# Kernel tuning notes

Measured on AMD Instinct MI355X. Metric: run time of the kernel, lower is better.

## Reference

```python
import jax, jax.numpy as jnp
import numpy as np

LORA_DIM = 16          # hard-coded in module
LORA_TOKEN_INDEX = 1   # lora_dim*layer_sequence + 1 with layer_sequence=0
B, S, D, H = 4, 2048, 1024, 4096  # num_hiddens = 4*num_input (forced by view())


def setup_inputs() -> dict:
    key = jax.random.key(0)
    ks = jax.random.split(key, 6)
    x = jax.random.normal(ks[0], (B, S, D), dtype=jnp.float32)
    W1 = jax.random.normal(ks[1], (H, D), dtype=jnp.float32) * 0.02
    b1 = jnp.zeros((H,), dtype=jnp.float32)
    W2 = jax.random.normal(ks[2], (D, H), dtype=jnp.float32) * 0.02
    b2 = jnp.zeros((D,), dtype=jnp.float32)
    scale = jnp.asarray(0.001, dtype=jnp.float32)  # nn.Parameter(torch.tensor(0.001))
    return {"x": x, "W1": W1, "b1": b1, "W2": W2, "b2": b2, "scale": scale}


def reference(x, W1, b1, W2, b2, scale):
    Bx, Sx, Dx = x.shape
    Hx = W1.shape[0]  # = 4*Dx
    # 16 lora tokens starting at LORA_TOKEN_INDEX
    lt = jax.lax.dynamic_slice_in_dim(x, LORA_TOKEN_INDEX, LORA_DIM, axis=1)
    even = lt[:, ::2, :]  # (B, 8, D)
    odd = lt[:, 1::2, :]  # (B, 8, D)
    # per-sample low-rank weight updates:
    # result_multiplication[b,k] = outer(even[b,k], odd[b,k]) (D,D)
    # matrix1 = first 4 blocks stacked -> (B, 4D, D); matrix2 = last 4 reshaped -> (B, D, 4D)
    m1 = (even[:, :4, :, None] * odd[:, :4, None, :]).reshape(Bx, Hx, Dx)
    m2 = (even[:, 4:, :, None] * odd[:, 4:, None, :]).reshape(Bx, Dx, Hx)
    # x @ (W1 + scale*m1)^T + b1, fused without repeating W1 per batch
    h = jnp.einsum('bsd,hd->bsh', x, W1) + scale * jnp.einsum('bsd,bhd->bsh', x, m1) + b1
    h = jax.nn.gelu(h, approximate=False)  # torch nn.GELU default = exact erf
    out = jnp.einsum('bsh,oh->bso', h, W2) + scale * jnp.einsum('bsh,boh->bso', h, m2) + b2
    return out
```

## Files before the change

kernel.cpp:

```cpp
#include <hip/hip_runtime.h>
#include <cstdint>
#include <cstddef>

#define MROWS 8192
#define DDIM  1024
#define HDIM  4096

typedef __bf16 bf16x8 __attribute__((ext_vector_type(8)));
typedef float  f32x4  __attribute__((ext_vector_type(4)));

typedef __attribute__((address_space(1))) void* as1_vp;
typedef __attribute__((address_space(3))) void* as3_vp;

__device__ __forceinline__ unsigned short f2bf(float f) {
  unsigned int u = __builtin_bit_cast(unsigned int, f);
  u += 0x7fffu + ((u >> 16) & 1u);
  return (unsigned short)(u >> 16);
}
__device__ __forceinline__ float bf2f(unsigned short h) {
  return __builtin_bit_cast(float, (unsigned int)h << 16);
}

__device__ __forceinline__ float fast_gelu(float x) {
  float x3 = x * x * x;
  float z = 0.7978845608028654f * x + 0.03567740814f * x3;
  float e = __builtin_amdgcn_exp2f(z * 2.8853900817779268f);
  float t = 1.0f - 2.0f * __builtin_amdgcn_rcpf(e + 1.0f);
  return 0.5f * x * (1.0f + t);
}

__device__ __forceinline__ void gld_lds16(const unsigned short* g, unsigned short* lds) {
  __builtin_amdgcn_global_load_lds((as1_vp)(uintptr_t)g, (as3_vp)lds, 16, 0, 0);
}

__global__ __launch_bounds__(256) void pre_kernel(
    const float* __restrict__ x, const float* __restrict__ w1,
    const float* __restrict__ w2, unsigned short* __restrict__ xb,
    unsigned short* __restrict__ w1b, unsigned short* __restrict__ w2b,
    float* __restrict__ p1) {
  if (blockIdx.x < 8192) {
    int i = blockIdx.x * 256 + threadIdx.x;
    const float* src; unsigned short* dst; int off;
    if (i < 1048576) { src = w1; dst = w1b; off = i; }
    else             { src = w2; dst = w2b; off = i - 1048576; }
    float4 v = ((const float4*)src)[off];
    ushort4 o;
    o.x = f2bf(v.x); o.y = f2bf(v.y); o.z = f2bf(v.z); o.w = f2bf(v.w);
    ((ushort4*)dst)[off] = o;
    return;
  }
  const int bid = blockIdx.x - 8192;
  const int wave = threadIdx.x >> 6, lane = threadIdx.x & 63;
  const int m = bid * 4 + wave;
  const int b = m >> 11;
  const float4* xrow4 = (const float4*)(x + (size_t)m * DDIM);
  const float4* od4   = (const float4*)(x + ((size_t)b * 2048 + 2) * DDIM);
  ushort4* xbrow4 = (ushort4*)(xb + (size_t)m * DDIM);
  float a0 = 0.f, a1 = 0.f, a2 = 0.f, a3 = 0.f;
#pragma unroll
  for (int it = 0; it < 4; ++it) {
    int g = it * 64 + lane;
    float4 v = xrow4[g];
    ushort4 o; o.x = f2bf(v.x); o.y = f2bf(v.y); o.z = f2bf(v.z); o.w = f2bf(v.w);
    xbrow4[g] = o;
    float4 o0 = od4[g];
    float4 o1 = od4[512 + g];
    float4 o2 = od4[1024 + g];
    float4 o3 = od4[1536 + g];
    a0 += v.x * o0.x + v.y * o0.y + v.z * o0.z + v.w * o0.w;
    a1 += v.x * o1.x + v.y * o1.y + v.z * o1.z + v.w * o1.w;
    a2 += v.x * o2.x + v.y * o2.y + v.z * o2.z + v.w * o2.w;
    a3 += v.x * o3.x + v.y * o3.y + v.z * o3.z + v.w * o3.w;
  }
#pragma unroll
  for (int off = 32; off > 0; off >>= 1) {
    a0 += __shfl_down(a0, off);
    a1 += __shfl_down(a1, off);
    a2 += __shfl_down(a2, off);
    a3 += __shfl_down(a3, off);
  }
  if (lane == 0) {
    float4 r; r.x = a0; r.y = a1; r.z = a2; r.w = a3;
    ((float4*)p1)[m] = r;
  }
}

__global__ __launch_bounds__(256) void p2_kernel(const unsigned short* __restrict__ hact,
                                                 const float* __restrict__ x,
                                                 float* __restrict__ p2) {
  const int wave = threadIdx.x >> 6, lane = threadIdx.x & 63;
  const int m = blockIdx.x * 4 + wave;
  const int b = m >> 11;
  const ushort4* hrow4 = (const ushort4*)(hact + (size_t)m * HDIM);
  const float4* od4    = (const float4*)(x + ((size_t)b * 2048 + 10) * DDIM);
  float acc[4][4] = {{0.f}};
#pragma unroll
  for (int it = 0; it < 4; ++it) {
    int g = it * 64 + lane;
    float h[4][4];
#pragma unroll
    for (int r = 0; r < 4; ++r) {
      ushort4 hv = hrow4[r * 256 + g];
      h[r][0] = bf2f(hv.x); h[r][1] = bf2f(hv.y); h[r][2] = bf2f(hv.z); h[r][3] = bf2f(hv.w);
    }
#pragma unroll
    for (int i = 0; i < 4; ++i) {
      float4 ov = od4[i * 512 + g];
#pragma unroll
      for (int r = 0; r < 4; ++r)
        acc[i][r] += ov.x * h[r][0] + ov.y * h[r][1] + ov.z * h[r][2] + ov.w * h[r][3];
    }
  }
#pragma unroll
  for (int i = 0; i < 4; ++i)
#pragma unroll
    for (int r = 0; r < 4; ++r)
#pragma unroll
      for (int off = 32; off > 0; off >>= 1)
        acc[i][r] += __shfl_down(acc[i][r], off);
  if (lane == 0) {
#pragma unroll
    for (int i = 0; i < 4; ++i) {
      float4 v; v.x = acc[i][0]; v.y = acc[i][1]; v.z = acc[i][2]; v.w = acc[i][3];
      ((float4*)(p2 + (size_t)m * 16))[i] = v;
    }
  }
}

__device__ __forceinline__ void gemm_bt_tile(const unsigned short* __restrict__ A,
                                             const unsigned short* __restrict__ B,
                                             const int ld, const int Kloop,
                                             const int m0, const int n0,
                                             unsigned short* As, unsigned short* Bs,
                                             f32x4 acc[4][4]) {
  const int tid  = threadIdx.x;
  const int wave = tid >> 6;
  const int lane = tid & 63;
  const int quad = lane >> 4;
  const int l16  = lane & 15;
  const int wm   = (wave >> 1) * 64;
  const int wn   = (wave & 1) * 64;

  const unsigned short* ga[4]; const unsigned short* gb[4];
#pragma unroll
  for (int s = 0; s < 4; ++s) {
    int idx = wave * 256 + s * 64 + lane;
    int r = idx >> 3, sl = idx & 7;
    int c = (sl - r) & 7;
    ga[s] = A + (size_t)(m0 + r) * ld + c * 8;
    gb[s] = B + (size_t)(n0 + r) * ld + c * 8;
  }

  for (int k0 = 0; k0 < Kloop; k0 += 64) {
    __syncthreads();
#pragma unroll
    for (int s = 0; s < 4; ++s) gld_lds16(ga[s] + k0, As + (wave * 4 + s) * 512);
#pragma unroll
    for (int s = 0; s < 4; ++s) gld_lds16(gb[s] + k0, Bs + (wave * 4 + s) * 512);
    __syncthreads();
#pragma unroll
    for (int kk = 0; kk < 64; kk += 32) {
      bf16x8 a[4], b[4];
      const int cbase = (kk >> 3) + quad;
#pragma unroll
      for (int i = 0; i < 4; ++i) {
        const int ra = wm + i * 16 + l16;
        const int rb = wn + i * 16 + l16;
        a[i] = *(const bf16x8*)(As + ra * 64 + ((cbase + ra) & 7) * 8);
        b[i] = *(const bf16x8*)(Bs + rb * 64 + ((cbase + rb) & 7) * 8);
      }
#pragma unroll
      for (int i = 0; i < 4; ++i)
#pragma unroll
        for (int j = 0; j < 4; ++j)
          acc[i][j] = __builtin_amdgcn_mfma_f32_16x16x32_bf16(a[i], b[j], acc[i][j], 0, 0, 0);
    }
  }
}

__global__ __launch_bounds__(256) void gemm1_kernel(
    const unsigned short* __restrict__ xb, const unsigned short* __restrict__ w1b,
    const float* __restrict__ x, const float* __restrict__ b1,
    const float* __restrict__ p1, const float* __restrict__ scale_p,
    unsigned short* __restrict__ hact) {
  __shared__ __align__(16) unsigned short As[128 * 64];
  __shared__ __align__(16) unsigned short Bs[128 * 64];
  const int id = blockIdx.x;
  const int xcd = id & 7, w = id >> 3;
  const int m0 = (xcd * 8 + (w & 7)) * 128;
  const int n0 = (w >> 3) * 128;
  f32x4 acc[4][4];
  const f32x4 z = {0.f, 0.f, 0.f, 0.f};
#pragma unroll
  for (int i = 0; i < 4; ++i)
#pragma unroll
    for (int j = 0; j < 4; ++j) acc[i][j] = z;

  gemm_bt_tile(xb, w1b, DDIM, DDIM, m0, n0, As, Bs, acc);

  const int tid = threadIdx.x;
  const int wave = tid >> 6, lane = tid & 63, quad = lane >> 4, l16 = lane & 15;
  const int wm = (wave >> 1) * 64, wn = (wave & 1) * 64;
  const float sc = scale_p[0];
  const int bidx = m0 >> 11;
  const int i1 = (n0 + wn) >> 10;
  const float* exrow = x + ((size_t)(bidx * 2048 + 1 + 2 * i1)) * DDIM;

  float exv[4], b1v[4]; int nn[4];
#pragma unroll
  for (int j = 0; j < 4; ++j) {
    nn[j]  = n0 + wn + j * 16 + l16;
    exv[j] = exrow[nn[j] & 1023];
    b1v[j] = b1[nn[j]];
  }
#pragma unroll
  for (int i = 0; i < 4; ++i) {
#pragma unroll
    for (int r = 0; r < 4; ++r) {
      const int m = m0 + wm + i * 16 + quad * 4 + r;
      const float pv = p1[(size_t)m * 4 + i1] * sc;
#pragma unroll
      for (int j = 0; j < 4; ++j) {
        float v = acc[i][j][r] + b1v[j] + pv * exv[j];
        hact[(size_t)m * HDIM + nn[j]] = f2bf(fast_gelu(v));
      }
    }
  }
}

__global__ __launch_bounds__(256) void gemm2_kernel(
    const unsigned short* __restrict__ hact, const unsigned short* __restrict__ w2b,
    const float* __restrict__ x, const float* __restrict__ b2,
    const float* __restrict__ p2, const float* __restrict__ scale_p,
    float* __restrict__ out) {
  __shared__ __align__(16) unsigned short As[128 * 64];
  __shared__ __align__(16) unsigned short Bs[128 * 64];
  const int id = blockIdx.x;
  const int xcd = id & 7, w = id >> 3;
  const int m0 = (xcd * 8 + (w >> 3)) * 128;
  const int n0 = (w & 7) * 128;
  f32x4 acc[4][4];
  const f32x4 z = {0.f, 0.f, 0.f, 0.f};
#pragma unroll
  for (int i = 0; i < 4; ++i)
#pragma unroll
    for (int j = 0; j < 4; ++j) acc[i][j] = z;

  gemm_bt_tile(hact, w2b, HDIM, HDIM, m0, n0, As, Bs, acc);

  const int tid = threadIdx.x;
  const int wave = tid >> 6, lane = tid & 63, quad = lane >> 4, l16 = lane & 15;
  const int wm = (wave >> 1) * 64, wn = (wave & 1) * 64;
  const float sc = scale_p[0];
  const int bidx = m0 >> 11;
  const int i2 = (n0 + wn) >> 8;
  const float* evrow = x + ((size_t)(bidx * 2048 + 9 + 2 * i2)) * DDIM;

  float4 ev[4]; float b2v[4]; int nn[4];
#pragma unroll
  for (int j = 0; j < 4; ++j) {
    nn[j] = n0 + wn + j * 16 + l16;
    ev[j]  = *(const float4*)(evrow + 4 * (nn[j] & 255));
    b2v[j] = b2[nn[j]];
  }
#pragma unroll
  for (int i = 0; i < 4; ++i) {
#pragma unroll
    for (int r = 0; r < 4; ++r) {
      const int m = m0 + wm + i * 16 + quad * 4 + r;
      const float4 pv = *(const float4*)(p2 + (size_t)m * 16 + i2 * 4);
#pragma unroll
      for (int j = 0; j < 4; ++j) {
        float lora = ev[j].x * pv.x + ev[j].y * pv.y + ev[j].z * pv.z + ev[j].w * pv.w;
        out[(size_t)m * DDIM + nn[j]] = acc[i][j][r] + b2v[j] + sc * lora;
      }
    }
  }
}

extern "C" void kernel_launch(void* const* d_in, const int* in_sizes, int n_in,
                              void* d_out, int out_size, void* d_ws, size_t ws_size,
                              hipStream_t stream) {
  const float* x     = (const float*)d_in[0];
  const float* W1    = (const float*)d_in[1];
  const float* b1    = (const float*)d_in[2];
  const float* W2    = (const float*)d_in[3];
  const float* b2    = (const float*)d_in[4];
  const float* scale = (const float*)d_in[5];
  float* out = (float*)d_out;

  char* ws = (char*)d_ws;
  unsigned short* xb   = (unsigned short*)(ws);
  unsigned short* w1b  = (unsigned short*)(ws + 16777216);
  unsigned short* w2b  = (unsigned short*)(ws + 25165824);
  unsigned short* hact = (unsigned short*)(ws + 33554432);
  float*          p1   = (float*)(ws + 100663296);
  float*          p2   = (float*)(ws + 100794368);

  pre_kernel<<<dim3(10240), dim3(256), 0, stream>>>(x, W1, W2, xb, w1b, w2b, p1);
  gemm1_kernel<<<dim3(2048), dim3(256), 0, stream>>>(xb, w1b, x, b1, p1, scale, hact);
  p2_kernel<<<dim3(2048), dim3(256), 0, stream>>>(hact, x, p2);
  gemm2_kernel<<<dim3(512), dim3(256), 0, stream>>>(hact, w2b, x, b2, p2, scale, out);
}
```

Measured before the change: 284.1 us.

## Fuse p2 low-rank projection into gemm1 epilogue and widen gemm2 K-tile

Removes the separate p2 kernel, which re-read the whole hidden activation buffer. The p2 dot products are now computed in the gemm1 epilogue from the fp32 GELU outputs and accumulated into p2 with atomics, which pre_kernel zeroes first. Gemm2 is also rewritten inline with a 128-wide K tile using 64 KB of LDS, halving the number of barrier-separated K iterations. The cost is atomic traffic in gemm1, and fewer resident blocks per CU in gemm2 because of the larger LDS footprint.

New measurement: 387.5 us. 1.36x slower.

```diff
diff --git a/kernel.cpp b/kernel.cpp
--- a/kernel.cpp
+++ b/kernel.cpp
@@ -37,7 +37,13 @@
     const float* __restrict__ x, const float* __restrict__ w1,
     const float* __restrict__ w2, unsigned short* __restrict__ xb,
     unsigned short* __restrict__ w1b, unsigned short* __restrict__ w2b,
-    float* __restrict__ p1) {
+    float* __restrict__ p1, float* __restrict__ p2) {
+  if (blockIdx.x >= 10240) {
+    int i = (blockIdx.x - 10240) * 256 + threadIdx.x;
+    float4 z; z.x = 0.f; z.y = 0.f; z.z = 0.f; z.w = 0.f;
+    ((float4*)p2)[i] = z;
+    return;
+  }
   if (blockIdx.x < 8192) {
     int i = blockIdx.x * 256 + threadIdx.x;
     const float* src; unsigned short* dst; int off;
@@ -85,54 +91,12 @@
   }
 }
 
-__global__ __launch_bounds__(256) void p2_kernel(const unsigned short* __restrict__ hact,
-                                                 const float* __restrict__ x,
-                                                 float* __restrict__ p2) {
-  const int wave = threadIdx.x >> 6, lane = threadIdx.x & 63;
-  const int m = blockIdx.x * 4 + wave;
-  const int b = m >> 11;
-  const ushort4* hrow4 = (const ushort4*)(hact + (size_t)m * HDIM);
-  const float4* od4    = (const float4*)(x + ((size_t)b * 2048 + 10) * DDIM);
-  float acc[4][4] = {{0.f}};
-#pragma unroll
-  for (int it = 0; it < 4; ++it) {
-    int g = it * 64 + lane;
-    float h[4][4];
-#pragma unroll
-    for (int r = 0; r < 4; ++r) {
-      ushort4 hv = hrow4[r * 256 + g];
-      h[r][0] = bf2f(hv.x); h[r][1] = bf2f(hv.y); h[r][2] = bf2f(hv.z); h[r][3] = bf2f(hv.w);
-    }
-#pragma unroll
-    for (int i = 0; i < 4; ++i) {
-      float4 ov = od4[i * 512 + g];
-#pragma unroll
-      for (int r = 0; r < 4; ++r)
-        acc[i][r] += ov.x * h[r][0] + ov.y * h[r][1] + ov.z * h[r][2] + ov.w * h[r][3];
-    }
-  }
-#pragma unroll
-  for (int i = 0; i < 4; ++i)
-#pragma unroll
-    for (int r = 0; r < 4; ++r)
-#pragma unroll
-      for (int off = 32; off > 0; off >>= 1)
-        acc[i][r] += __shfl_down(acc[i][r], off);
-  if (lane == 0) {
-#pragma unroll
-    for (int i = 0; i < 4; ++i) {
-      float4 v; v.x = acc[i][0]; v.y = acc[i][1]; v.z = acc[i][2]; v.w = acc[i][3];
-      ((float4*)(p2 + (size_t)m * 16))[i] = v;
-    }
-  }
-}
-
-__device__ __forceinline__ void gemm_bt_tile(const unsigned short* __restrict__ A,
-                                             const unsigned short* __restrict__ B,
-                                             const int ld, const int Kloop,
-                                             const int m0, const int n0,
-                                             unsigned short* As, unsigned short* Bs,
-                                             f32x4 acc[4][4]) {
+__device__ __forceinline__ void gemm_bt_tile64(const unsigned short* __restrict__ A,
+                                               const unsigned short* __restrict__ B,
+                                               const int ld, const int Kloop,
+                                               const int m0, const int n0,
+                                               unsigned short* As, unsigned short* Bs,
+                                               f32x4 acc[4][4]) {
   const int tid  = threadIdx.x;
   const int wave = tid >> 6;
   const int lane = tid & 63;
@@ -182,7 +146,7 @@
     const unsigned short* __restrict__ xb, const unsigned short* __restrict__ w1b,
     const float* __restrict__ x, const float* __restrict__ b1,
     const float* __restrict__ p1, const float* __restrict__ scale_p,
-    unsigned short* __restrict__ hact) {
+    unsigned short* __restrict__ hact, float* __restrict__ p2) {
   __shared__ __align__(16) unsigned short As[128 * 64];
   __shared__ __align__(16) unsigned short Bs[128 * 64];
   const int id = blockIdx.x;
@@ -196,7 +160,7 @@
 #pragma unroll
     for (int j = 0; j < 4; ++j) acc[i][j] = z;
 
-  gemm_bt_tile(xb, w1b, DDIM, DDIM, m0, n0, As, Bs, acc);
+  gemm_bt_tile64(xb, w1b, DDIM, DDIM, m0, n0, As, Bs, acc);
 
   const int tid = threadIdx.x;
   const int wave = tid >> 6, lane = tid & 63, quad = lane >> 4, l16 = lane & 15;
@@ -206,12 +170,18 @@
   const int i1 = (n0 + wn) >> 10;
   const float* exrow = x + ((size_t)(bidx * 2048 + 1 + 2 * i1)) * DDIM;
 
-  float exv[4], b1v[4]; int nn[4];
+  const int seg = n0 >> 10;
+  const int cb  = (n0 & 1023) + wn;
+  float exv[4], b1v[4], odv[4][4]; int nn[4];
 #pragma unroll
   for (int j = 0; j < 4; ++j) {
     nn[j]  = n0 + wn + j * 16 + l16;
     exv[j] = exrow[nn[j] & 1023];
     b1v[j] = b1[nn[j]];
+    const int c = cb + j * 16 + l16;
+#pragma unroll
+    for (int t = 0; t < 4; ++t)
+      odv[t][j] = x[((size_t)(bidx * 2048 + 10 + 2 * t)) * DDIM + c];
   }
 #pragma unroll
   for (int i = 0; i < 4; ++i) {
@@ -219,10 +189,28 @@
     for (int r = 0; r < 4; ++r) {
       const int m = m0 + wm + i * 16 + quad * 4 + r;
       const float pv = p1[(size_t)m * 4 + i1] * sc;
+      float tok[4] = {0.f, 0.f, 0.f, 0.f};
 #pragma unroll
       for (int j = 0; j < 4; ++j) {
         float v = acc[i][j][r] + b1v[j] + pv * exv[j];
-        hact[(size_t)m * HDIM + nn[j]] = f2bf(fast_gelu(v));
+        float g = fast_gelu(v);
+        hact[(size_t)m * HDIM + nn[j]] = f2bf(g);
+#pragma unroll
+        for (int t = 0; t < 4; ++t) tok[t] += g * odv[t][j];
+      }
+#pragma unroll
+      for (int t = 0; t < 4; ++t) {
+        tok[t] += __shfl_xor(tok[t], 1);
+        tok[t] += __shfl_xor(tok[t], 2);
+        tok[t] += __shfl_xor(tok[t], 4);
+        tok[t] += __shfl_xor(tok[t], 8);
+      }
+      if (l16 == 0) {
+        float* pp = p2 + (size_t)m * 16 + seg;
+        atomicAdd(pp + 0,  tok[0]);
+        atomicAdd(pp + 4,  tok[1]);
+        atomicAdd(pp + 8,  tok[2]);
+        atomicAdd(pp + 12, tok[3]);
       }
     }
   }
@@ -233,24 +221,58 @@
     const float* __restrict__ x, const float* __restrict__ b2,
     const float* __restrict__ p2, const float* __restrict__ scale_p,
     float* __restrict__ out) {
-  __shared__ __align__(16) unsigned short As[128 * 64];
-  __shared__ __align__(16) unsigned short Bs[128 * 64];
+  __shared__ __align__(16) unsigned short As[128 * 128];
+  __shared__ __align__(16) unsigned short Bs[128 * 128];
   const int id = blockIdx.x;
   const int xcd = id & 7, w = id >> 3;
   const int m0 = (xcd * 8 + (w >> 3)) * 128;
   const int n0 = (w & 7) * 128;
-  f32x4 acc[4][4];
-  const f32x4 z = {0.f, 0.f, 0.f, 0.f};
-#pragma unroll
-  for (int i = 0; i < 4; ++i)
-#pragma unroll
-    for (int j = 0; j < 4; ++j) acc[i][j] = z;
-
-  gemm_bt_tile(hact, w2b, HDIM, HDIM, m0, n0, As, Bs, acc);
-
   const int tid = threadIdx.x;
   const int wave = tid >> 6, lane = tid & 63, quad = lane >> 4, l16 = lane & 15;
   const int wm = (wave >> 1) * 64, wn = (wave & 1) * 64;
+  f32x4 acc[4][4];
+  const f32x4 z = {0.f, 0.f, 0.f, 0.f};
+#pragma unroll
+  for (int i = 0; i < 4; ++i)
+#pragma unroll
+    for (int j = 0; j < 4; ++j) acc[i][j] = z;
+
+  const unsigned short* ga[8]; const unsigned short* gb[8];
+#pragma unroll
+  for (int s = 0; s < 8; ++s) {
+    int idx = wave * 512 + s * 64 + lane;
+    int r = idx >> 4, sl = idx & 15;
+    int c = (sl - r) & 15;
+    ga[s] = hact + (size_t)(m0 + r) * HDIM + c * 8;
+    gb[s] = w2b  + (size_t)(n0 + r) * HDIM + c * 8;
+  }
+
+  for (int k0 = 0; k0 < HDIM; k0 += 128) {
+    __syncthreads();
+#pragma unroll
+    for (int s = 0; s < 8; ++s) gld_lds16(ga[s] + k0, As + (wave * 8 + s) * 512);
+#pragma unroll
+    for (int s = 0; s < 8; ++s) gld_lds16(gb[s] + k0, Bs + (wave * 8 + s) * 512);
+    __syncthreads();
+#pragma unroll
+    for (int kk = 0; kk < 128; kk += 32) {
+      bf16x8 a[4], b[4];
+      const int cbase = (kk >> 3) + quad;
+#pragma unroll
+      for (int i = 0; i < 4; ++i) {
+        const int ra = wm + i * 16 + l16;
+        const int rb = wn + i * 16 + l16;
+        a[i] = *(const bf16x8*)(As + ra * 128 + ((cbase + ra) & 15) * 8);
+        b[i] = *(const bf16x8*)(Bs + rb * 128 + ((cbase + rb) & 15) * 8);
+      }
+#pragma unroll
+      for (int i = 0; i < 4; ++i)
+#pragma unroll
+        for (int j = 0; j < 4; ++j)
+          acc[i][j] = __builtin_amdgcn_mfma_f32_16x16x32_bf16(a[i], b[j], acc[i][j], 0, 0, 0);
+    }
+  }
+
   const float sc = scale_p[0];
   const int bidx = m0 >> 11;
   const int i2 = (n0 + wn) >> 8;
@@ -297,8 +319,7 @@
   float*          p1   = (float*)(ws + 100663296);
   float*          p2   = (float*)(ws + 100794368);
 
-  pre_kernel<<<dim3(10240), dim3(256), 0, stream>>>(x, W1, W2, xb, w1b, w2b, p1);
-  gemm1_kernel<<<dim3(2048), dim3(256), 0, stream>>>(xb, w1b, x, b1, p1, scale, hact);
-  p2_kernel<<<dim3(2048), dim3(256), 0, stream>>>(hact, x, p2);
+  pre_kernel<<<dim3(10368), dim3(256), 0, stream>>>(x, W1, W2, xb, w1b, w2b, p1, p2);
+  gemm1_kernel<<<dim3(2048), dim3(256), 0, stream>>>(xb, w1b, x, b1, p1, scale, hact, p2);
   gemm2_kernel<<<dim3(512), dim3(256), 0, stream>>>(hact, w2b, x, b2, p2, scale, out);
 }
```
